# Kernel tuning notes

Measured on AMD Instinct MI355X. Metric: run time of the kernel, lower is better.

The kernel has to match this reference:

```python
import jax, jax.numpy as jnp
import numpy as np

D_MODEL = 2048
HEADS = 32
HEAD_DIM = 64   # D_MODEL // HEADS
STATE = 256
KCONV = 4
CHUNK = 64
EPS = 1e-5
CONV_DIM = D_MODEL + 2 * STATE          # 2560 (n_groups=1)
PROJ = D_MODEL + CONV_DIM + HEADS       # 4640 (z | xBC | dt)
BATCH, SEQ = 2, 2048


def rmsnorm(x, w, eps=EPS):
    return x * jax.lax.rsqrt(jnp.mean(x * x, axis=-1, keepdims=True) + eps) * w


def setup_inputs() -> dict:
    key = jax.random.key(0)
    ks = jax.random.split(key, 8)
    x = jax.random.normal(ks[0], (BATCH, SEQ, D_MODEL), jnp.float32)
    norm_w = jnp.ones((D_MODEL,), jnp.float32)
    w_in = jax.random.normal(ks[1], (D_MODEL, PROJ), jnp.float32) * 0.02
    conv_w = jax.random.normal(ks[2], (CONV_DIM, KCONV), jnp.float32) * 0.2
    conv_b = jnp.zeros((CONV_DIM,), jnp.float32)
    # HF-style dt init: softplus(dt_bias) uniform-log in [1e-3, 1e-1]
    dt0 = jnp.exp(jax.random.uniform(ks[3], (HEADS,)) * (np.log(0.1) - np.log(0.001)) + np.log(0.001))
    dt_bias = dt0 + jnp.log(-jnp.expm1(-dt0))
    A_log = jnp.log(jnp.arange(1, HEADS + 1, dtype=jnp.float32))
    D_skip = jnp.ones((HEADS,), jnp.float32)
    gnorm_w = jnp.ones((D_MODEL,), jnp.float32)
    w_out = jax.random.normal(ks[4], (D_MODEL, D_MODEL), jnp.float32) * 0.02
    wo_w = jax.random.normal(ks[5], (D_MODEL, D_MODEL), jnp.float32) * 0.02
    return {"x": x, "norm_w": norm_w, "w_in": w_in, "conv_w": conv_w, "conv_b": conv_b,
            "dt_bias": dt_bias, "A_log": A_log, "D_skip": D_skip, "gnorm_w": gnorm_w,
            "w_out": w_out, "wo_w": wo_w}


def reference(x, norm_w, w_in, conv_w, conv_b, dt_bias, A_log, D_skip, gnorm_w, w_out, wo_w):
    b, L, _ = x.shape
    nc = L // CHUNK
    # pre-RMSNorm
    xn = rmsnorm(x, norm_w)
    # in_proj and split: z | xBC | dt
    proj = xn @ w_in
    z = proj[..., :D_MODEL]
    xBC = proj[..., D_MODEL:D_MODEL + CONV_DIM]
    dt = proj[..., D_MODEL + CONV_DIM:]                      # [b,L,H]
    # causal depthwise conv1d (kernel 4) + SiLU
    xp = jnp.pad(xBC, ((0, 0), (KCONV - 1, 0), (0, 0)))
    conv = conv_b + sum(xp[:, k:k + L] * conv_w[:, k] for k in range(KCONV))
    conv = jax.nn.silu(conv)
    xs = conv[..., :D_MODEL].reshape(b, L, HEADS, HEAD_DIM)  # SSM input
    Bm = conv[..., D_MODEL:D_MODEL + STATE]                  # [b,L,N] (n_groups=1)
    Cm = conv[..., D_MODEL + STATE:]                         # [b,L,N]
    dt = jax.nn.softplus(dt + dt_bias)                       # [b,L,H], >0
    A = -jnp.exp(A_log)                                      # [H]
    # ---- Mamba2 chunked selective scan (chunk_size=64) ----
    def ck(a):
        return a.reshape(b, nc, CHUNK, *a.shape[2:])
    xs_c, dt_c, B_c, C_c = ck(xs), ck(dt), ck(Bm), ck(Cm)
    Adt = dt_c * A                                           # [b,c,l,h] (<=0)
    Acs = jnp.cumsum(Adt, axis=2)
    # intra-chunk (diagonal blocks)
    seg = Acs[:, :, :, None, :] - Acs[:, :, None, :, :]      # [b,c,l,s,h]
    idx = jnp.arange(CHUNK)
    mask = (idx[:, None] >= idx[None, :])[None, None, :, :, None]
    Lmat = jnp.where(mask, jnp.exp(seg), 0.0)                # [b,c,l,s,h]
    CB = jnp.einsum('bcln,bcsn->bcls', C_c, B_c)
    xt = xs_c * dt_c[..., None]                              # [b,c,l,h,p]
    Y_diag = jnp.einsum('bclsh,bcshp->bclhp', CB[..., None] * Lmat, xt)
    # chunk-final states
    decay_states = jnp.exp(Acs[:, :, -1:, :] - Acs)          # [b,c,l,h]
    states = jnp.einsum('bcln,bclh,bclhp->bchpn', B_c, decay_states, xt)
    # inter-chunk recurrence (scan over nc chunks only)
    chunk_decay = jnp.exp(Acs[:, :, -1, :])                  # [b,c,h]
    def step(S, inp):
        dec, st = inp
        return S * dec[:, :, None, None] + st, S
    S0 = jnp.zeros((b, HEADS, HEAD_DIM, STATE), x.dtype)
    _, prev = jax.lax.scan(step, S0, (jnp.moveaxis(chunk_decay, 1, 0), jnp.moveaxis(states, 1, 0)))
    prev = jnp.moveaxis(prev, 0, 1)                          # [b,c,h,p,n] state at chunk start
    Y_off = jnp.einsum('bcln,bchpn,bclh->bclhp', C_c, prev, jnp.exp(Acs))
    y = (Y_diag + Y_off).reshape(b, L, HEADS, HEAD_DIM) + D_skip[None, None, :, None] * xs
    y = y.reshape(b, L, D_MODEL)
    # gated RMSNorm, out_proj, then wo
    y = rmsnorm(y * jax.nn.silu(z), gnorm_w)
    return (y @ w_out) @ wo_w
```

## Files before the change

kernel.cpp:

```cpp
#include <hip/hip_runtime.h>
#include <math.h>

#define D_MODEL 2048
#define HEADS 32
#define HEAD_DIM 64
#define STATE 256
#define KCONV 4
#define CHUNK 64
#define NC 32
#define SEQL 2048
#define BATCHN 2
#define CONV_DIMN 2560
#define PROJ_DIM 4640
#define PROJB_W 4608
#define EPSF 1e-5f
#define BL (BATCHN * SEQL)

typedef __attribute__((ext_vector_type(8))) short short8;
typedef __attribute__((ext_vector_type(4))) short short4v;
typedef __attribute__((ext_vector_type(4))) float f32x4;

__device__ __forceinline__ short f2bf(float f) {
  unsigned u = __builtin_bit_cast(unsigned, f);
  u = (u + 0x7fffu + ((u >> 16) & 1u)) >> 16;
  return (short)u;
}
__device__ __forceinline__ float b2f(short s) {
  unsigned u = ((unsigned)(unsigned short)s) << 16;
  return __builtin_bit_cast(float, u);
}
__device__ __forceinline__ void gld16(const void* g, void* l) {
  __builtin_amdgcn_global_load_lds((const __attribute__((address_space(1))) unsigned int*)g,
                                   (__attribute__((address_space(3))) unsigned int*)l,
                                   16, 0, 0);
}

__global__ __launch_bounds__(256) void transpose_bf16_k(const float* __restrict__ W,
                                                        short* __restrict__ WT,
                                                        int K, int ncols, int stride) {
  __shared__ float tile[32][33];
  int bn = blockIdx.x * 32, bk = blockIdx.y * 32;
  int tx = threadIdx.x & 31, ty = threadIdx.x >> 5;
  #pragma unroll
  for (int i = 0; i < 32; i += 8) {
    int k = bk + ty + i, n = bn + tx;
    tile[ty + i][tx] = (n < ncols) ? W[(size_t)k * stride + n] : 0.f;
  }
  __syncthreads();
  #pragma unroll
  for (int i = 0; i < 32; i += 8) {
    int n = bn + ty + i, k = bk + tx;
    WT[(size_t)n * K + k] = f2bf(tile[tx][ty + i]);
  }
}

__global__ __launch_bounds__(256) void dt_gemm_k(const float* __restrict__ x,
                                                 const float* __restrict__ norm_w,
                                                 const float* __restrict__ w_in,
                                                 short* __restrict__ xnb,
                                                 float* __restrict__ dtraw) {
  int row = blockIdx.x;
  int t = threadIdx.x;
  __shared__ float sx[D_MODEL];
  __shared__ float red[8][32];
  __shared__ float sred[4];
  const float4* x4 = (const float4*)(x + (size_t)row * D_MODEL);
  const float4* nw4 = (const float4*)norm_w;
  float ss = 0.f;
  for (int i = t; i < D_MODEL / 4; i += 256) {
    float4 v = x4[i];
    ss += v.x * v.x + v.y * v.y + v.z * v.z + v.w * v.w;
    float4 nw = nw4[i];
    float4 pv; pv.x = v.x * nw.x; pv.y = v.y * nw.y; pv.z = v.z * nw.z; pv.w = v.w * nw.w;
    ((float4*)sx)[i] = pv;
  }
  #pragma unroll
  for (int off = 32; off > 0; off >>= 1) ss += __shfl_down(ss, off);
  if ((t & 63) == 0) sred[t >> 6] = ss;
  __syncthreads();
  float tot = sred[0] + sred[1] + sred[2] + sred[3];
  float scale = rsqrtf(tot / (float)D_MODEL + EPSF);
  {
    float4 a = ((const float4*)sx)[2 * t], b = ((const float4*)sx)[2 * t + 1];
    short tmp[8];
    tmp[0] = f2bf(a.x * scale); tmp[1] = f2bf(a.y * scale);
    tmp[2] = f2bf(a.z * scale); tmp[3] = f2bf(a.w * scale);
    tmp[4] = f2bf(b.x * scale); tmp[5] = f2bf(b.y * scale);
    tmp[6] = f2bf(b.z * scale); tmp[7] = f2bf(b.w * scale);
    *(int4*)(xnb + (size_t)row * D_MODEL + t * 8) = *(int4*)tmp;
  }
  int h = t & 31, sl = t >> 5;
  float acc = 0.f;
  for (int k = sl * 256; k < sl * 256 + 256; k++)
    acc += sx[k] * w_in[(size_t)k * PROJ_DIM + (D_MODEL + CONV_DIMN) + h];
  red[sl][h] = acc;
  __syncthreads();
  if (t < 32) {
    float s = 0.f;
    #pragma unroll
    for (int i = 0; i < 8; i++) s += red[i][t];
    dtraw[(size_t)row * HEADS + t] = s * scale;
  }
}

template<bool BF16OUT>
__global__ __launch_bounds__(512, 4) void gemm128_k(const short* __restrict__ A,
                                                    const short* __restrict__ BT,
                                                    void* __restrict__ Cout,
                                                    int M, int N, int K) {
  constexpr int ABUF = 128 * 32;
  constexpr int BUFS = ABUF + 8192;
  constexpr int LPT = 3;
  __shared__ short lds[3 * BUFS];

  const int t = threadIdx.x;
  const int lane = t & 63, w = t >> 6;
  const int mr = lane & 15, q = lane >> 4;
  const int cq8 = (q ^ ((mr >> 1) & 3)) * 8;
  const int stj = ((lane & 3) ^ ((lane >> 3) & 3)) * 8;
  const int str = lane >> 2;

  const int nbx = N >> 8;
  const int nwg = nbx * (M >> 7);
  const int cpx = nwg >> 3;
  const int bid = blockIdx.x;
  const int swz = (bid & 7) * cpx + (bid >> 3);
  const int bx = swz % nbx, by = swz / nbx;
  const int m0 = by * 128, n0 = bx * 256;

  const int NT = K >> 5;
  f32x4 acc[8][2] = {};

  auto STAGE = [&](int tile, int buf) {
    short* dst = &lds[buf * BUFS];
    const int kb = tile * 32 + stj;
    gld16(A + (size_t)(m0 + w * 16 + str) * K + kb, dst + w * 512);
    const short* gB = BT + (size_t)(n0 + w * 32 + str) * K + kb;
    short* dB = dst + ABUF + w * 1024;
    gld16(gB, dB);
    gld16(gB + (size_t)16 * K, dB + 512);
  };

  STAGE(0, 0); STAGE(1, 1);
  asm volatile("s_waitcnt vmcnt(%0)" :: "n"(LPT) : "memory");
  __builtin_amdgcn_s_barrier();

  int bufc = 0;
  for (int tt = 0; tt < NT; ++tt) {
    const short* sA = &lds[bufc * BUFS];
    const short* sB = sA + ABUF;
    if (tt + 2 < NT) STAGE(tt + 2, bufc >= 1 ? bufc - 1 : 2);
    short8 af[4], bfr[2];
    #pragma unroll
    for (int ni = 0; ni < 2; ni++)
      bfr[ni] = *(const short8*)&sB[(w * 32 + ni * 16 + mr) * 32 + cq8];
    #pragma unroll
    for (int mi = 0; mi < 4; mi++)
      af[mi] = *(const short8*)&sA[(mi * 16 + mr) * 32 + cq8];
    __builtin_amdgcn_s_setprio(1);
    #pragma unroll
    for (int mi = 0; mi < 4; mi++)
      #pragma unroll
      for (int ni = 0; ni < 2; ni++)
        acc[mi][ni] = __builtin_amdgcn_mfma_f32_16x16x32_bf16(af[mi], bfr[ni], acc[mi][ni], 0, 0, 0);
    __builtin_amdgcn_s_setprio(0);
    #pragma unroll
    for (int mi = 0; mi < 4; mi++)
      af[mi] = *(const short8*)&sA[(64 + mi * 16 + mr) * 32 + cq8];
    __builtin_amdgcn_s_setprio(1);
    #pragma unroll
    for (int mi = 0; mi < 4; mi++)
      #pragma unroll
      for (int ni = 0; ni < 2; ni++)
        acc[4 + mi][ni] = __builtin_amdgcn_mfma_f32_16x16x32_bf16(af[mi], bfr[ni], acc[4 + mi][ni], 0, 0, 0);
    __builtin_amdgcn_s_setprio(0);
    __builtin_amdgcn_sched_barrier(0);
    if (tt + 2 < NT) asm volatile("s_waitcnt vmcnt(%0)" :: "n"(LPT) : "memory");
    else             asm volatile("s_waitcnt vmcnt(0)" ::: "memory");
    __builtin_amdgcn_s_barrier();
    bufc = (bufc == 2) ? 0 : bufc + 1;
  }

  #pragma unroll
  for (int mi = 0; mi < 8; mi++)
    #pragma unroll
    for (int ni = 0; ni < 2; ni++) {
      const int gm = m0 + mi * 16 + q * 4;
      const int gn = n0 + w * 32 + ni * 16 + mr;
      #pragma unroll
      for (int r = 0; r < 4; r++) {
        if (BF16OUT) ((short*)Cout)[(size_t)(gm + r) * N + gn] = f2bf(acc[mi][ni][r]);
        else         ((float*)Cout)[(size_t)(gm + r) * N + gn] = acc[mi][ni][r];
      }
    }
}

__global__ __launch_bounds__(256) void conv_silu_k(const short* __restrict__ projb,
                                                   const float* __restrict__ cw,
                                                   const float* __restrict__ cb,
                                                   short* __restrict__ out) {
  int idx = blockIdx.x * 256 + threadIdx.x;
  int ci = idx % (CONV_DIMN / 8);
  int bt = idx / (CONV_DIMN / 8);
  int t = bt & (SEQL - 1);
  int b = bt >> 11;
  int c = ci * 8;
  float4 w4[8];
  #pragma unroll
  for (int j = 0; j < 8; j++) w4[j] = ((const float4*)cw)[c + j];
  float acc[8];
  {
    float4 b0 = ((const float4*)(cb + c))[0], b1 = ((const float4*)(cb + c))[1];
    acc[0] = b0.x; acc[1] = b0.y; acc[2] = b0.z; acc[3] = b0.w;
    acc[4] = b1.x; acc[5] = b1.y; acc[6] = b1.z; acc[7] = b1.w;
  }
  #pragma unroll
  for (int k = 0; k < KCONV; k++) {
    int tt = t - (KCONV - 1) + k;
    if (tt < 0) continue;
    short8 v = *(const short8*)&projb[((size_t)(b * SEQL + tt)) * PROJB_W + D_MODEL + c];
    #pragma unroll
    for (int j = 0; j < 8; j++) {
      float wv = (k == 0) ? w4[j].x : (k == 1) ? w4[j].y : (k == 2) ? w4[j].z : w4[j].w;
      acc[j] += b2f(v[j]) * wv;
    }
  }
  short o[8];
  #pragma unroll
  for (int j = 0; j < 8; j++) o[j] = f2bf(acc[j] / (1.f + expf(-acc[j])));
  *(int4*)&out[(size_t)bt * CONV_DIMN + c] = *(int4*)o;
}

__global__ __launch_bounds__(256) void dt_acs_k(const float* __restrict__ dtraw,
                                                const float* __restrict__ dt_bias,
                                                const float* __restrict__ A_log,
                                                float* __restrict__ dtb, float* __restrict__ acsb) {
  int bc = blockIdx.x;
  int b = bc / NC, c = bc % NC;
  int t = threadIdx.x;
  int l = t & 63, w = t >> 6;
  size_t base = ((size_t)(b * SEQL + c * CHUNK + l)) * HEADS;
  #pragma unroll
  for (int i = 0; i < 8; i++) {
    int h = w * 8 + i;
    float raw = dtraw[base + h] + dt_bias[h];
    float dt = raw > 20.f ? raw : log1pf(expf(raw));
    float adt = -expf(A_log[h]) * dt;
    float cs = adt;
    #pragma unroll
    for (int off = 1; off < 64; off <<= 1) {
      float v = __shfl_up(cs, off);
      if (l >= off) cs += v;
    }
    dtb[base + h] = dt;
    acsb[base + h] = cs;
  }
}

__global__ __launch_bounds__(256) void cb_k(const short* __restrict__ convb,
                                            short* __restrict__ CB) {
  int bc = blockIdx.x;
  int b = bc / NC, c = bc % NC;
  __shared__ float sC[64][65];
  __shared__ float sB[64][65];
  int t = threadIdx.x;
  int s = t & 63;
  int lb = (t >> 6) * 16;
  float acc[16] = {};
  size_t rowb = ((size_t)(b * SEQL + c * CHUNK)) * CONV_DIMN;
  for (int nt = 0; nt < 4; nt++) {
    __syncthreads();
    #pragma unroll
    for (int i = 0; i < 16; i++) {
      int e = t + 256 * i;
      int r = e >> 6, col = e & 63;
      sC[r][col] = b2f(convb[rowb + (size_t)r * CONV_DIMN + (D_MODEL + STATE) + nt * 64 + col]);
      sB[r][col] = b2f(convb[rowb + (size_t)r * CONV_DIMN + D_MODEL + nt * 64 + col]);
    }
    __syncthreads();
    for (int n = 0; n < 64; n++) {
      float bv = sB[s][n];
      #pragma unroll
      for (int j = 0; j < 16; j++) acc[j] += sC[lb + j][n] * bv;
    }
  }
  size_t ob = ((size_t)bc) * 64 * 64;
  #pragma unroll
  for (int j = 0; j < 16; j++) CB[ob + (size_t)(lb + j) * 64 + s] = f2bf(acc[j]);
}

__global__ __launch_bounds__(256) void chunk_states_k(const short* __restrict__ convb,
                                                      const float* __restrict__ dtb,
                                                      const float* __restrict__ acsb,
                                                      short* __restrict__ G0,
                                                      short* __restrict__ G1) {
  int blk = blockIdx.x & 1023;
  int b = blockIdx.x >> 10;
  short* G = b ? G1 : G0;
  int h = blk & 31, c = blk >> 5;
  __shared__ __align__(16) short sXT[64][72];
  __shared__ __align__(16) short sBT[256][72];
  __shared__ float swt[64];
  int t = threadIdx.x;
  size_t rowb = ((size_t)(b * SEQL + c * CHUNK)) * CONV_DIMN;
  size_t ab = ((size_t)(b * SEQL + c * CHUNK)) * HEADS;
  if (t < 64) {
    float a = acsb[ab + (size_t)t * HEADS + h];
    float alast = acsb[ab + (size_t)63 * HEADS + h];
    swt[t] = expf(alast - a) * dtb[ab + (size_t)t * HEADS + h];
  }
  __syncthreads();
  #pragma unroll
  for (int i = 0; i < 4; i++) {
    int e = t + 256 * i;
    int l = e >> 4, p4 = (e & 15) * 4;
    short4v v = *(const short4v*)&convb[rowb + (size_t)l * CONV_DIMN + h * HEAD_DIM + p4];
    float wt = swt[l];
    short vv[4] = {v.x, v.y, v.z, v.w};
    #pragma unroll
    for (int j = 0; j < 4; j++) {
      int p = p4 + j;
      sXT[p][((((l >> 3) ^ ((p >> 2) & 7)) << 3) | (l & 7))] = f2bf(b2f(vv[j]) * wt);
    }
  }
  #pragma unroll
  for (int i = 0; i < 16; i++) {
    int e = t + 256 * i;
    int l = e >> 6, n4 = (e & 63) * 4;
    short4v v = *(const short4v*)&convb[rowb + (size_t)l * CONV_DIMN + D_MODEL + n4];
    short vv[4] = {v.x, v.y, v.z, v.w};
    #pragma unroll
    for (int j = 0; j < 4; j++) {
      int n = n4 + j;
      sBT[n][((((l >> 3) ^ ((n >> 2) & 7)) << 3) | (l & 7))] = vv[j];
    }
  }
  __syncthreads();
  int lane = t & 63, w = t >> 6;
  int mr = lane & 15, q = lane >> 4;
  f32x4 acc[4][4] = {};
  #pragma unroll
  for (int ks = 0; ks < 2; ks++) {
    short8 af[4], bfr[4];
    #pragma unroll
    for (int mi = 0; mi < 4; mi++) {
      int p = mi * 16 + mr;
      af[mi] = *(const short8*)&sXT[p][(((ks * 4 + q) ^ ((p >> 2) & 7)) << 3)];
    }
    #pragma unroll
    for (int ni = 0; ni < 4; ni++) {
      int n = w * 64 + ni * 16 + mr;
      bfr[ni] = *(const short8*)&sBT[n][(((ks * 4 + q) ^ ((n >> 2) & 7)) << 3)];
    }
    #pragma unroll
    for (int mi = 0; mi < 4; mi++)
      #pragma unroll
      for (int ni = 0; ni < 4; ni++)
        acc[mi][ni] = __builtin_amdgcn_mfma_f32_16x16x32_bf16(af[mi], bfr[ni], acc[mi][ni], 0, 0, 0);
  }
  size_t gb = (size_t)blk * (64 * 256);
  #pragma unroll
  for (int mi = 0; mi < 4; mi++)
    #pragma unroll
    for (int ni = 0; ni < 4; ni++)
      #pragma unroll
      for (int r = 0; r < 4; r++)
        G[gb + (size_t)(mi * 16 + q * 4 + r) * 256 + w * 64 + ni * 16 + mr] = f2bf(acc[mi][ni][r]);
}

__global__ __launch_bounds__(256) void scan_states_k(short* __restrict__ G0,
                                                     short* __restrict__ G1,
                                                     const float* __restrict__ acsb) {
  int gid = blockIdx.x * 256 + threadIdx.x;
  int b = gid >> 16;
  int tid = gid & 65535;
  short* G = b ? G1 : G0;
  int n8 = tid & 31, p = (tid >> 5) & 63, h = tid >> 11;
  float S[8] = {};
  for (int c = 0; c < NC; c++) {
    size_t base = (((size_t)(c * HEADS + h) * 64) + p) * 256 + n8 * 8;
    short gs[8];
    *(int4*)gs = *(const int4*)&G[base];
    short ws8[8];
    #pragma unroll
    for (int j = 0; j < 8; j++) ws8[j] = f2bf(S[j]);
    *(int4*)&G[base] = *(int4*)ws8;
    float dec = expf(acsb[((size_t)(b * SEQL + c * CHUNK + 63)) * HEADS + h]);
    #pragma unroll
    for (int j = 0; j < 8; j++) S[j] = S[j] * dec + b2f(gs[j]);
  }
}

__global__ __launch_bounds__(256) void y_fused_k(const short* __restrict__ convb,
                                                 const short* __restrict__ CBb,
                                                 const short* __restrict__ G0,
                                                 const short* __restrict__ G1,
                                                 const float* __restrict__ dtb,
                                                 const float* __restrict__ acsb,
                                                 const float* __restrict__ D_skip,
                                                 float* __restrict__ Y) {
  int blk = blockIdx.x & 1023;
  int b = blockIdx.x >> 10;
  const short* G = b ? G1 : G0;
  int h = blk & 31, c = blk >> 5;
  __shared__ __align__(16) short sM[64][72];
  __shared__ __align__(16) short sXT[64][72];
  __shared__ float sacs[64], sdt[64], sea[64];
  int t = threadIdx.x;
  int lane = t & 63, w = t >> 6;
  size_t rowb = ((size_t)(b * SEQL + c * CHUNK)) * CONV_DIMN;
  size_t ab = ((size_t)(b * SEQL + c * CHUNK)) * HEADS;
  size_t cbbase = ((size_t)(b * NC + c)) * 64 * 64;
  if (t < 64) {
    float a = acsb[ab + (size_t)t * HEADS + h];
    sacs[t] = a;
    sea[t] = expf(a);
    sdt[t] = dtb[ab + (size_t)t * HEADS + h];
  }
  __syncthreads();
  #pragma unroll
  for (int i = 0; i < 16; i++) {
    int e = t + 256 * i;
    int r = e >> 6, col = e & 63;
    float m = 0.f;
    if (col <= r)
      m = b2f(CBb[cbbase + (size_t)r * 64 + col]) * expf(sacs[r] - sacs[col]) * sdt[col];
    sM[r][col] = f2bf(m);
  }
  #pragma unroll
  for (int i = 0; i < 4; i++) {
    int e = t + 256 * i;
    int l = e >> 4, p4 = (e & 15) * 4;
    short4v v = *(const short4v*)&convb[rowb + (size_t)l * CONV_DIMN + h * HEAD_DIM + p4];
    short vv[4] = {v.x, v.y, v.z, v.w};
    #pragma unroll
    for (int j = 0; j < 4; j++) {
      int p = p4 + j;
      sXT[p][((((l >> 3) ^ ((p >> 2) & 7)) << 3) | (l & 7))] = vv[j];
    }
  }
  __syncthreads();
  int mr = lane & 15, q = lane >> 4;
  int wm = (w & 1) * 32, wn = (w >> 1) * 32;
  f32x4 acc1[2][2] = {}, acc2[2][2] = {};
  #pragma unroll
  for (int ks = 0; ks < 2; ks++) {
    short8 af[2], bfr[2];
    #pragma unroll
    for (int mi = 0; mi < 2; mi++)
      af[mi] = *(const short8*)&sM[wm + mi * 16 + mr][ks * 32 + q * 8];
    #pragma unroll
    for (int ni = 0; ni < 2; ni++) {
      int p = wn + ni * 16 + mr;
      bfr[ni] = *(const short8*)&sXT[p][(((ks * 4 + q) ^ ((p >> 2) & 7)) << 3)];
    }
    #pragma unroll
    for (int mi = 0; mi < 2; mi++)
      #pragma unroll
      for (int ni = 0; ni < 2; ni++)
        acc1[mi][ni] = __builtin_amdgcn_mfma_f32_16x16x32_bf16(af[mi], bfr[ni], acc1[mi][ni], 0, 0, 0);
  }
  const short* Crow = convb + rowb + (D_MODEL + STATE);
  size_t gbase = (size_t)blk * (64 * 256);
  #pragma unroll
  for (int st = 0; st < 8; st++) {
    short8 af[2], bfr[2];
    #pragma unroll
    for (int mi = 0; mi < 2; mi++) {
      int l = wm + mi * 16 + mr;
      af[mi] = *(const short8*)&Crow[(size_t)l * CONV_DIMN + st * 32 + q * 8];
    }
    #pragma unroll
    for (int ni = 0; ni < 2; ni++) {
      int p = wn + ni * 16 + mr;
      bfr[ni] = *(const short8*)&G[gbase + (size_t)p * 256 + st * 32 + q * 8];
    }
    #pragma unroll
    for (int mi = 0; mi < 2; mi++)
      #pragma unroll
      for (int ni = 0; ni < 2; ni++)
        acc2[mi][ni] = __builtin_amdgcn_mfma_f32_16x16x32_bf16(af[mi], bfr[ni], acc2[mi][ni], 0, 0, 0);
  }
  float dsk = D_skip[h];
  size_t ybase = ((size_t)(b * SEQL + c * CHUNK)) * D_MODEL + h * HEAD_DIM;
  #pragma unroll
  for (int mi = 0; mi < 2; mi++)
    #pragma unroll
    for (int ni = 0; ni < 2; ni++) {
      int p = wn + ni * 16 + mr;
      #pragma unroll
      for (int r = 0; r < 4; r++) {
        int l = wm + mi * 16 + q * 4 + r;
        float xsv = b2f(sXT[p][((((l >> 3) ^ ((p >> 2) & 7)) << 3) | (l & 7))]);
        Y[ybase + (size_t)l * D_MODEL + p] =
            acc1[mi][ni][r] + sea[l] * acc2[mi][ni][r] + dsk * xsv;
      }
    }
}

__global__ __launch_bounds__(256) void gated_norm_bf16_k(const float* __restrict__ Y,
                                                         const short* __restrict__ projb,
                                                         const float* __restrict__ gw,
                                                         short* __restrict__ out) {
  int row = blockIdx.x;
  int t = threadIdx.x;
  const float4* y4 = (const float4*)(Y + (size_t)row * D_MODEL);
  float4 ya = y4[2 * t], yb = y4[2 * t + 1];
  short zt[8];
  *(int4*)zt = *(const int4*)(projb + (size_t)row * PROJB_W + t * 8);
  float g[8];
  float yv[8] = {ya.x, ya.y, ya.z, ya.w, yb.x, yb.y, yb.z, yb.w};
  float ss = 0.f;
  #pragma unroll
  for (int i = 0; i < 8; i++) {
    float z = b2f(zt[i]);
    g[i] = yv[i] * (z / (1.f + expf(-z)));
    ss += g[i] * g[i];
  }
  #pragma unroll
  for (int off = 32; off > 0; off >>= 1) ss += __shfl_down(ss, off);
  __shared__ float ws_[4];
  if ((t & 63) == 0) ws_[t >> 6] = ss;
  __syncthreads();
  float tot = ws_[0] + ws_[1] + ws_[2] + ws_[3];
  float scale = rsqrtf(tot / (float)D_MODEL + EPSF);
  const float4* g4 = (const float4*)gw;
  float4 wa = g4[2 * t], wb = g4[2 * t + 1];
  float wv[8] = {wa.x, wa.y, wa.z, wa.w, wb.x, wb.y, wb.z, wb.w};
  short tmp[8];
  #pragma unroll
  for (int i = 0; i < 8; i++) tmp[i] = f2bf(g[i] * scale * wv[i]);
  *(int4*)(out + (size_t)row * D_MODEL + t * 8) = *(int4*)tmp;
}

extern "C" void kernel_launch(void* const* d_in, const int* in_sizes, int n_in,
                              void* d_out, int out_size, void* d_ws, size_t ws_size,
                              hipStream_t stream) {
  const float* x       = (const float*)d_in[0];
  const float* norm_w  = (const float*)d_in[1];
  const float* w_in    = (const float*)d_in[2];
  const float* conv_w  = (const float*)d_in[3];
  const float* conv_b  = (const float*)d_in[4];
  const float* dt_bias = (const float*)d_in[5];
  const float* A_log   = (const float*)d_in[6];
  const float* D_skip  = (const float*)d_in[7];
  const float* gnorm_w = (const float*)d_in[8];
  const float* w_out   = (const float*)d_in[9];
  const float* wo_w    = (const float*)d_in[10];
  float* out = (float*)d_out;

  float* ws    = (float*)d_ws;
  short* xnb   = (short*)ws;
  short* w_inT = (short*)(ws + 4194304);
  short* projb = (short*)(ws + 8912896);
  short* convb = (short*)(ws + 18350080);
  float* dtraw = ws + 23592960;
  float* dtb   = ws + 23724032;
  float* acsb  = ws + 23855104;
  short* CBb   = (short*)(ws + 23986176);
  float* Yb    = ws + 24117248;
  short* w_outT= (short*)(ws + 32505856);
  short* wo_wT = (short*)(ws + 34603008);
  short* G0    = (short*)ws;
  short* G1    = (short*)out;
  short* Yg    = convb;
  short* t1b   = (short*)ws;

  dt_gemm_k<<<BL, 256, 0, stream>>>(x, norm_w, w_in, xnb, dtraw);
  transpose_bf16_k<<<dim3(PROJB_W / 32, D_MODEL / 32), 256, 0, stream>>>(w_in, w_inT, D_MODEL, PROJB_W, PROJ_DIM);
  transpose_bf16_k<<<dim3(D_MODEL / 32, D_MODEL / 32), 256, 0, stream>>>(w_out, w_outT, D_MODEL, D_MODEL, D_MODEL);
  transpose_bf16_k<<<dim3(D_MODEL / 32, D_MODEL / 32), 256, 0, stream>>>(wo_w, wo_wT, D_MODEL, D_MODEL, D_MODEL);
  gemm128_k<true><<<(BL / 128) * (PROJB_W / 256), 512, 0, stream>>>(xnb, w_inT, projb, BL, PROJB_W, D_MODEL);
  conv_silu_k<<<(BL * (CONV_DIMN / 8)) / 256, 256, 0, stream>>>(projb, conv_w, conv_b, convb);
  dt_acs_k<<<BATCHN * NC, 256, 0, stream>>>(dtraw, dt_bias, A_log, dtb, acsb);
  cb_k<<<BATCHN * NC, 256, 0, stream>>>(convb, CBb);
  chunk_states_k<<<BATCHN * NC * HEADS, 256, 0, stream>>>(convb, dtb, acsb, G0, G1);
  scan_states_k<<<512, 256, 0, stream>>>(G0, G1, acsb);
  y_fused_k<<<BATCHN * NC * HEADS, 256, 0, stream>>>(convb, CBb, G0, G1, dtb, acsb, D_skip, Yb);
  gated_norm_bf16_k<<<BL, 256, 0, stream>>>(Yb, projb, gnorm_w, Yg);
  gemm128_k<true><<<(BL / 128) * (D_MODEL / 256), 512, 0, stream>>>(Yg, w_outT, t1b, BL, D_MODEL, D_MODEL);
  gemm128_k<false><<<(BL / 128) * (D_MODEL / 256), 512, 0, stream>>>(t1b, wo_wT, out, BL, D_MODEL, D_MODEL);
}
```

Baseline: 606.2 us.

## Restructure bf16 GEMM to 256x128 tiles with 4 waves in 2x2 layout

The GEMM kernel goes from 512 threads covering 128x256 tiles to 256 threads covering 256x128 tiles. Its four waves form a 2x2 grid, and each wave computes a 128x64 sub-tile with 32 MFMA accumulators. The aim is more MFMA work per LDS fragment load and fewer waves per tile, which should improve operand reuse from shared memory. In exchange each thread holds many more accumulator registers, the launch bound drops to 2 blocks, occupancy may fall, and there are fewer workgroups for the grid to spread across CUs.

```diff
diff --git a/kernel.cpp b/kernel.cpp
--- a/kernel.cpp
+++ b/kernel.cpp
@@ -104,13 +104,13 @@
 }
 
 template<bool BF16OUT>
-__global__ __launch_bounds__(512, 4) void gemm128_k(const short* __restrict__ A,
+__global__ __launch_bounds__(256, 2) void gemm_tw_k(const short* __restrict__ A,
                                                     const short* __restrict__ BT,
                                                     void* __restrict__ Cout,
                                                     int M, int N, int K) {
-  constexpr int ABUF = 128 * 32;
-  constexpr int BUFS = ABUF + 8192;
-  constexpr int LPT = 3;
+  constexpr int ABUF = 256 * 32;
+  constexpr int BUFS = ABUF + 128 * 32;
+  constexpr int LPT = 6;
   __shared__ short lds[3 * BUFS];
 
   const int t = threadIdx.x;
@@ -119,26 +119,30 @@
   const int cq8 = (q ^ ((mr >> 1) & 3)) * 8;
   const int stj = ((lane & 3) ^ ((lane >> 3) & 3)) * 8;
   const int str = lane >> 2;
-
-  const int nbx = N >> 8;
-  const int nwg = nbx * (M >> 7);
+  const int wm = w & 1, wn = w >> 1;
+
+  const int nbx = N >> 7;
+  const int nwg = nbx * (M >> 8);
   const int cpx = nwg >> 3;
   const int bid = blockIdx.x;
   const int swz = (bid & 7) * cpx + (bid >> 3);
   const int bx = swz % nbx, by = swz / nbx;
-  const int m0 = by * 128, n0 = bx * 256;
+  const int m0 = by * 256, n0 = bx * 128;
 
   const int NT = K >> 5;
-  f32x4 acc[8][2] = {};
+  f32x4 acc[8][4] = {};
 
   auto STAGE = [&](int tile, int buf) {
     short* dst = &lds[buf * BUFS];
     const int kb = tile * 32 + stj;
-    gld16(A + (size_t)(m0 + w * 16 + str) * K + kb, dst + w * 512);
-    const short* gB = BT + (size_t)(n0 + w * 32 + str) * K + kb;
-    short* dB = dst + ABUF + w * 1024;
-    gld16(gB, dB);
-    gld16(gB + (size_t)16 * K, dB + 512);
+    #pragma unroll
+    for (int cc = 0; cc < 4; cc++)
+      gld16(A + (size_t)(m0 + w * 64 + cc * 16 + str) * K + kb,
+            dst + (w * 64 + cc * 16) * 32);
+    #pragma unroll
+    for (int cc = 0; cc < 2; cc++)
+      gld16(BT + (size_t)(n0 + w * 32 + cc * 16 + str) * K + kb,
+            dst + ABUF + (w * 32 + cc * 16) * 32);
   };
 
   STAGE(0, 0); STAGE(1, 1);
@@ -150,28 +154,28 @@
     const short* sA = &lds[bufc * BUFS];
     const short* sB = sA + ABUF;
     if (tt + 2 < NT) STAGE(tt + 2, bufc >= 1 ? bufc - 1 : 2);
-    short8 af[4], bfr[2];
-    #pragma unroll
-    for (int ni = 0; ni < 2; ni++)
-      bfr[ni] = *(const short8*)&sB[(w * 32 + ni * 16 + mr) * 32 + cq8];
+    short8 af[4], bfr[4];
+    #pragma unroll
+    for (int ni = 0; ni < 4; ni++)
+      bfr[ni] = *(const short8*)&sB[(wn * 64 + ni * 16 + mr) * 32 + cq8];
     #pragma unroll
     for (int mi = 0; mi < 4; mi++)
-      af[mi] = *(const short8*)&sA[(mi * 16 + mr) * 32 + cq8];
+      af[mi] = *(const short8*)&sA[(wm * 128 + mi * 16 + mr) * 32 + cq8];
     __builtin_amdgcn_s_setprio(1);
     #pragma unroll
     for (int mi = 0; mi < 4; mi++)
       #pragma unroll
-      for (int ni = 0; ni < 2; ni++)
+      for (int ni = 0; ni < 4; ni++)
         acc[mi][ni] = __builtin_amdgcn_mfma_f32_16x16x32_bf16(af[mi], bfr[ni], acc[mi][ni], 0, 0, 0);
     __builtin_amdgcn_s_setprio(0);
     #pragma unroll
     for (int mi = 0; mi < 4; mi++)
-      af[mi] = *(const short8*)&sA[(64 + mi * 16 + mr) * 32 + cq8];
+      af[mi] = *(const short8*)&sA[(wm * 128 + 64 + mi * 16 + mr) * 32 + cq8];
     __builtin_amdgcn_s_setprio(1);
     #pragma unroll
     for (int mi = 0; mi < 4; mi++)
       #pragma unroll
-      for (int ni = 0; ni < 2; ni++)
+      for (int ni = 0; ni < 4; ni++)
         acc[4 + mi][ni] = __builtin_amdgcn_mfma_f32_16x16x32_bf16(af[mi], bfr[ni], acc[4 + mi][ni], 0, 0, 0);
     __builtin_amdgcn_s_setprio(0);
     __builtin_amdgcn_sched_barrier(0);
@@ -184,13 +188,14 @@
   #pragma unroll
   for (int mi = 0; mi < 8; mi++)
     #pragma unroll
-    for (int ni = 0; ni < 2; ni++) {
-      const int gm = m0 + mi * 16 + q * 4;
-      const int gn = n0 + w * 32 + ni * 16 + mr;
+    for (int ni = 0; ni < 4; ni++) {
+      const int gm = m0 + wm * 128 + ((mi & 3) + (mi >> 2) * 4) * 16 + ((mi >> 2) ? 64 - 64 : 0);
+      const int gmr = m0 + wm * 128 + (mi >> 2) * 64 + (mi & 3) * 16 + q * 4;
+      const int gn = n0 + wn * 64 + ni * 16 + mr;
       #pragma unroll
       for (int r = 0; r < 4; r++) {
-        if (BF16OUT) ((short*)Cout)[(size_t)(gm + r) * N + gn] = f2bf(acc[mi][ni][r]);
-        else         ((float*)Cout)[(size_t)(gm + r) * N + gn] = acc[mi][ni][r];
+        if (BF16OUT) ((short*)Cout)[(size_t)(gmr + r) * N + gn] = f2bf(acc[mi][ni][r]);
+        else         ((float*)Cout)[(size_t)(gmr + r) * N + gn] = acc[mi][ni][r];
       }
     }
 }
@@ -570,7 +575,7 @@
   transpose_bf16_k<<<dim3(PROJB_W / 32, D_MODEL / 32), 256, 0, stream>>>(w_in, w_inT, D_MODEL, PROJB_W, PROJ_DIM);
   transpose_bf16_k<<<dim3(D_MODEL / 32, D_MODEL / 32), 256, 0, stream>>>(w_out, w_outT, D_MODEL, D_MODEL, D_MODEL);
   transpose_bf16_k<<<dim3(D_MODEL / 32, D_MODEL / 32), 256, 0, stream>>>(wo_w, wo_wT, D_MODEL, D_MODEL, D_MODEL);
-  gemm128_k<true><<<(BL / 128) * (PROJB_W / 256), 512, 0, stream>>>(xnb, w_inT, projb, BL, PROJB_W, D_MODEL);
+  gemm_tw_k<true><<<(BL / 256) * (PROJB_W / 128), 256, 0, stream>>>(xnb, w_inT, projb, BL, PROJB_W, D_MODEL);
   conv_silu_k<<<(BL * (CONV_DIMN / 8)) / 256, 256, 0, stream>>>(projb, conv_w, conv_b, convb);
   dt_acs_k<<<BATCHN * NC, 256, 0, stream>>>(dtraw, dt_bias, A_log, dtb, acsb);
   cb_k<<<BATCHN * NC, 256, 0, stream>>>(convb, CBb);
@@ -578,6 +583,6 @@
   scan_states_k<<<512, 256, 0, stream>>>(G0, G1, acsb);
   y_fused_k<<<BATCHN * NC * HEADS, 256, 0, stream>>>(convb, CBb, G0, G1, dtb, acsb, D_skip, Yb);
   gated_norm_bf16_k<<<BL, 256, 0, stream>>>(Yb, projb, gnorm_w, Yg);
-  gemm128_k<true><<<(BL / 128) * (D_MODEL / 256), 512, 0, stream>>>(Yg, w_outT, t1b, BL, D_MODEL, D_MODEL);
-  gemm128_k<false><<<(BL / 128) * (D_MODEL / 256), 512, 0, stream>>>(t1b, wo_wT, out, BL, D_MODEL, D_MODEL);
-}
+  gemm_tw_k<true><<<(BL / 256) * (D_MODEL / 128), 256, 0, stream>>>(Yg, w_outT, t1b, BL, D_MODEL, D_MODEL);
+  gemm_tw_k<false><<<(BL / 256) * (D_MODEL / 128), 256, 0, stream>>>(t1b, wo_wT, out, BL, D_MODEL, D_MODEL);
+}
```

After: 606.4 us. Within noise of the previous version (+0.0%).
